# Kernel tuning notes

Measured on AMD Instinct MI355X. Metric: run time of the kernel, lower is better.

Reference implementation:

```python
import jax, jax.numpy as jnp
import numpy as np

HEADS = 8
DIM_HEAD = 64
DIM = 512
EPS = 1e-7  # module's self.eps, also used as LayerNorm eps


def _per_head_layernorm(t, w, b):
    # t: [b, h, n, d]; w, b: [h, d] (one LayerNorm per head, affine)
    mu = t.mean(axis=-1, keepdims=True)
    var = t.var(axis=-1, keepdims=True)  # biased, matches torch LayerNorm
    tn = (t - mu) * jax.lax.rsqrt(var + EPS)
    return tn * w[None, :, None, :] + b[None, :, None, :]


def setup_inputs() -> dict:
    key = jax.random.key(0)
    ks = jax.random.split(key, 4)
    inner = HEADS * DIM_HEAD
    return {
        "x": jax.random.normal(ks[0], (2, 2048, DIM), dtype=jnp.float32),
        "w_qkv": jax.random.normal(ks[1], (3 * inner, DIM), dtype=jnp.float32) * 0.02,
        "lnk_w": jnp.ones((HEADS, DIM_HEAD), dtype=jnp.float32),
        "lnk_b": jnp.zeros((HEADS, DIM_HEAD), dtype=jnp.float32),
        "lnv_w": jnp.ones((HEADS, DIM_HEAD), dtype=jnp.float32),
        "lnv_b": jnp.zeros((HEADS, DIM_HEAD), dtype=jnp.float32),
        "w_out": jax.random.normal(ks[2], (DIM, inner), dtype=jnp.float32) * 0.02,
        "b_out": jnp.zeros((DIM,), dtype=jnp.float32),
    }


def reference(x, w_qkv, lnk_w, lnk_b, lnv_w, lnv_b, w_out, b_out):
    b, n, _ = x.shape
    qkv = x @ w_qkv.T  # [b, n, 3*inner]
    q, k, v = jnp.split(qkv, 3, axis=-1)

    def split_heads(t):  # [b, n, h*d] -> [b, h, n, d]
        return t.reshape(b, n, HEADS, DIM_HEAD).transpose(0, 2, 1, 3)

    q, k, v = map(split_heads, (q, k, v))

    # per-head LayerNorm over dim_head on k and v
    k = _per_head_layernorm(k, lnk_w, lnk_b)
    v = _per_head_layernorm(v, lnv_w, lnv_b)

    # causal linear attention: prefix sums of k and of k-v outer products
    k_cum = jnp.cumsum(k, axis=2)  # [b, h, n, d]
    # scores: [b, h, n, d, e] prefix sums of outer products, scaled by 1/seq_len
    scores = jnp.cumsum(jnp.einsum('bhnd,bhne->bhnde', k, v), axis=2) / n
    d_inv = 1.0 / jnp.einsum('bhnd,bhnd->bhn', k_cum + EPS, q)  # [b, h, n]
    out = jnp.einsum('bhnd,bhnde,bhn->bhne', q, scores, d_inv)  # [b, h, n, e]

    out = out.transpose(0, 2, 1, 3).reshape(b, n, HEADS * DIM_HEAD)  # b n (h e)
    return out @ w_out.T + b_out
```

## Files before the change

kernel.cpp:

```cpp
#include <hip/hip_runtime.h>

constexpr int Bb   = 2;
constexpr int Nn   = 2048;
constexpr int Hh   = 8;
constexpr int Dd   = 64;
constexpr int Mm   = Bb * Nn;
constexpr int TQKV = 1536;
constexpr int INNER = Hh * Dd;
constexpr int CH   = 64;
constexpr int NCH  = Nn / CH;
constexpr int CSZ  = Dd * Dd + Dd;
constexpr float EPSF = 1e-7f;

typedef _Float16 half8 __attribute__((ext_vector_type(8)));
typedef _Float16 half4 __attribute__((ext_vector_type(4)));
typedef float f32x4 __attribute__((ext_vector_type(4)));

#define AS1(p) ((const __attribute__((address_space(1))) unsigned int*)(p))
#define AS3(p) ((__attribute__((address_space(3))) unsigned int*)(p))

__global__ __launch_bounds__(256) void gemm1_f32(
    const float* __restrict__ A, const float* __restrict__ B,
    float* __restrict__ C) {
  __shared__ float As[32][132];
  __shared__ float Bs[32][68];
  const int tid = threadIdx.x;
  const int tx = tid & 15, ty = tid >> 4;
  const int bm = blockIdx.y * 128, bn = blockIdx.x * 64;
  const int rowA = tid & 127, c4a = tid >> 7;
  const int rowB = tid & 63,  c4b = tid >> 6;

  float acc[8][4] = {};

  for (int k0 = 0; k0 < 512; k0 += 32) {
#pragma unroll
    for (int p = 0; p < 4; ++p) {
      int c4 = c4a + 2 * p;
      float4 fa = *(const float4*)(A + (size_t)(bm + rowA) * 512 + k0 + c4 * 4);
      As[c4 * 4 + 0][rowA] = fa.x; As[c4 * 4 + 1][rowA] = fa.y;
      As[c4 * 4 + 2][rowA] = fa.z; As[c4 * 4 + 3][rowA] = fa.w;
    }
#pragma unroll
    for (int p = 0; p < 2; ++p) {
      int c4 = c4b + 4 * p;
      float4 fb = *(const float4*)(B + (size_t)(bn + rowB) * 512 + k0 + c4 * 4);
      Bs[c4 * 4 + 0][rowB] = fb.x; Bs[c4 * 4 + 1][rowB] = fb.y;
      Bs[c4 * 4 + 2][rowB] = fb.z; Bs[c4 * 4 + 3][rowB] = fb.w;
    }
    __syncthreads();
#pragma unroll
    for (int kk = 0; kk < 32; ++kk) {
      float a[8], b[4];
      *(float4*)&a[0] = *(const float4*)&As[kk][ty * 8];
      *(float4*)&a[4] = *(const float4*)&As[kk][ty * 8 + 4];
      *(float4*)&b[0] = *(const float4*)&Bs[kk][tx * 4];
#pragma unroll
      for (int i = 0; i < 8; ++i)
#pragma unroll
        for (int j = 0; j < 4; ++j) acc[i][j] += a[i] * b[j];
    }
    __syncthreads();
  }

#pragma unroll
  for (int i = 0; i < 8; ++i) {
    size_t row = bm + ty * 8 + i;
    float4 r;
    r.x = acc[i][0]; r.y = acc[i][1]; r.z = acc[i][2]; r.w = acc[i][3];
    *(float4*)(C + row * (size_t)TQKV + bn + tx * 4) = r;
  }
}

__global__ __launch_bounds__(256) void split_f16_k(
    const float* __restrict__ s, _Float16* __restrict__ hi,
    _Float16* __restrict__ lo, int n4) {
  int i = blockIdx.x * 256 + threadIdx.x;
  if (i >= n4) return;
  float4 a = ((const float4*)s)[i];
  half4 h, l;
  float av[4] = {a.x, a.y, a.z, a.w};
#pragma unroll
  for (int j = 0; j < 4; ++j) {
    _Float16 hh = (_Float16)av[j];
    h[j] = hh;
    l[j] = (_Float16)((av[j] - (float)hh) * 2048.0f);
  }
  ((half4*)hi)[i] = h;
  ((half4*)lo)[i] = l;
}

__global__ __launch_bounds__(256) void gemm_split_nt(
    const _Float16* __restrict__ Ah, const _Float16* __restrict__ Al,
    const _Float16* __restrict__ Bh, const _Float16* __restrict__ Bl,
    const float* __restrict__ bias, float* __restrict__ C,
    int Ndim, int Kd) {
  constexpr int BM = 128, BN = 64, BK = 32;
  __shared__ _Float16 lds[(2 * BM + 2 * BN) * BK];
  constexpr int AHo = 0;
  constexpr int ALo = BM * BK;
  constexpr int BHo = 2 * BM * BK;
  constexpr int BLo = 2 * BM * BK + BN * BK;

  const int tid = threadIdx.x;
  const int wave = tid >> 6, lane = tid & 63;
  const int lq = lane >> 4, lm = lane & 15;
  const int bm = blockIdx.y * BM, bn = blockIdx.x * BN;

  f32x4 acc[2][4] = {};
  f32x4 corr[2][4] = {};

  const int nsteps = Kd >> 5;
  for (int ks = 0; ks < nsteps; ++ks) {
    const int k0 = ks * BK;
    for (int idx = wave; idx < 24; idx += 4) {
      int t, j;
      if (idx < 8)       { t = 0; j = idx; }
      else if (idx < 16) { t = 1; j = idx - 8; }
      else if (idx < 20) { t = 2; j = idx - 16; }
      else               { t = 3; j = idx - 20; }
      const int row = j * 16 + (lane >> 2);
      const _Float16* g;
      _Float16* l;
      if (t == 0)      { g = Ah + (size_t)(bm + row) * Kd; l = lds + AHo + j * 16 * BK; }
      else if (t == 1) { g = Al + (size_t)(bm + row) * Kd; l = lds + ALo + j * 16 * BK; }
      else if (t == 2) { g = Bh + (size_t)(bn + row) * Kd; l = lds + BHo + j * 16 * BK; }
      else             { g = Bl + (size_t)(bn + row) * Kd; l = lds + BLo + j * 16 * BK; }
      g += k0 + (lane & 3) * 8;
      __builtin_amdgcn_global_load_lds(AS1(g), AS3(l), 16, 0, 0);
    }
    __syncthreads();

    half8 ahf[2], alf[2], bhf[4], blf[4];
    const int mwo = wave * 32;
#pragma unroll
    for (int fi = 0; fi < 2; ++fi) {
      ahf[fi] = *(const half8*)&lds[AHo + (mwo + fi * 16 + lm) * BK + lq * 8];
      alf[fi] = *(const half8*)&lds[ALo + (mwo + fi * 16 + lm) * BK + lq * 8];
    }
#pragma unroll
    for (int fj = 0; fj < 4; ++fj) {
      bhf[fj] = *(const half8*)&lds[BHo + (fj * 16 + lm) * BK + lq * 8];
      blf[fj] = *(const half8*)&lds[BLo + (fj * 16 + lm) * BK + lq * 8];
    }
#pragma unroll
    for (int fi = 0; fi < 2; ++fi)
#pragma unroll
      for (int fj = 0; fj < 4; ++fj) {
        acc[fi][fj] = __builtin_amdgcn_mfma_f32_16x16x32_f16(
            ahf[fi], bhf[fj], acc[fi][fj], 0, 0, 0);
        corr[fi][fj] = __builtin_amdgcn_mfma_f32_16x16x32_f16(
            ahf[fi], blf[fj], corr[fi][fj], 0, 0, 0);
        corr[fi][fj] = __builtin_amdgcn_mfma_f32_16x16x32_f16(
            alf[fi], bhf[fj], corr[fi][fj], 0, 0, 0);
      }
    __syncthreads();
  }

#pragma unroll
  for (int fi = 0; fi < 2; ++fi) {
    const int m0 = bm + wave * 32 + fi * 16 + lq * 4;
#pragma unroll
    for (int fj = 0; fj < 4; ++fj) {
      const int n = bn + fj * 16 + lm;
      const float bb = bias ? bias[n] : 0.f;
      f32x4 v = acc[fi][fj];
      f32x4 cv = corr[fi][fj];
#pragma unroll
      for (int r = 0; r < 4; ++r)
        C[(size_t)(m0 + r) * Ndim + n] = v[r] + cv[r] * (1.0f / 2048.0f) + bb;
    }
  }
}

__global__ __launch_bounds__(256) void chunk_sums_ln(
    float* __restrict__ qkv, const float* __restrict__ lnk_w,
    const float* __restrict__ lnk_b, const float* __restrict__ lnv_w,
    const float* __restrict__ lnv_b, float* __restrict__ cbuf) {
  int blk = blockIdx.x;
  int c = blk % NCH;
  int bh = blk / NCH;
  int h = bh % Hh, b = bh / Hh;
  __shared__ float Ks[CH][68];
  __shared__ float Vs[CH][68];
  int tid = threadIdx.x;
  float* base = qkv + (size_t)(b * Nn + c * CH) * TQKV + h * Dd;
  for (int i = tid; i < CH * 16; i += 256) {
    int row = i >> 4, c4 = i & 15;
    *(float4*)&Ks[row][c4 * 4] =
        *(const float4*)(base + (size_t)row * TQKV + INNER + c4 * 4);
    *(float4*)&Vs[row][c4 * 4] =
        *(const float4*)(base + (size_t)row * TQKV + 2 * INNER + c4 * 4);
  }
  __syncthreads();

  if (tid < 128) {
    bool isv = tid >= 64;
    int row = tid & 63;
    float* R = isv ? &Vs[row][0] : &Ks[row][0];
    float s = 0.f, s2 = 0.f;
#pragma unroll
    for (int j = 0; j < 64; j += 4) {
      float4 v = *(const float4*)&R[j];
      s += v.x + v.y + v.z + v.w;
      s2 += v.x * v.x + v.y * v.y + v.z * v.z + v.w * v.w;
    }
    float mean = s * (1.f / 64.f);
    float var = s2 * (1.f / 64.f) - mean * mean;
    float inv = 1.0f / sqrtf(var + EPSF);
    const float* w = isv ? lnv_w : lnk_w;
    const float* bb = isv ? lnv_b : lnk_b;
#pragma unroll
    for (int j = 0; j < 64; ++j)
      R[j] = (R[j] - mean) * inv * w[h * Dd + j] + bb[h * Dd + j];
  }
  __syncthreads();

  for (int i = tid; i < CH * 16; i += 256) {
    int row = i >> 4, c4 = i & 15;
    *(float4*)(base + (size_t)row * TQKV + INNER + c4 * 4) =
        *(const float4*)&Ks[row][c4 * 4];
    *(float4*)(base + (size_t)row * TQKV + 2 * INNER + c4 * 4) =
        *(const float4*)&Vs[row][c4 * 4];
  }

  int d0 = (tid >> 4) * 4, e0 = (tid & 15) * 4;
  float acc[4][4] = {};
  float kc[4] = {0.f, 0.f, 0.f, 0.f};
  for (int n = 0; n < CH; ++n) {
    float4 kv = *(const float4*)&Ks[n][d0];
    float4 vv = *(const float4*)&Vs[n][e0];
    float ka[4] = {kv.x, kv.y, kv.z, kv.w};
    float va[4] = {vv.x, vv.y, vv.z, vv.w};
#pragma unroll
    for (int i = 0; i < 4; ++i)
#pragma unroll
      for (int j = 0; j < 4; ++j) acc[i][j] += ka[i] * va[j];
    if (e0 == 0) {
#pragma unroll
      for (int i = 0; i < 4; ++i) kc[i] += ka[i];
    }
  }
  float* out = cbuf + (size_t)blk * CSZ;
#pragma unroll
  for (int i = 0; i < 4; ++i) {
    float4 r;
    r.x = acc[i][0]; r.y = acc[i][1]; r.z = acc[i][2]; r.w = acc[i][3];
    *(float4*)(out + (size_t)(d0 + i) * Dd + e0) = r;
  }
  if (e0 == 0) {
#pragma unroll
    for (int i = 0; i < 4; ++i) out[Dd * Dd + d0 + i] = kc[i];
  }
}

__global__ __launch_bounds__(256) void chunk_prefix(float* __restrict__ cbuf) {
  int bh = blockIdx.y;
  int i = blockIdx.x * 256 + threadIdx.x;
  if (i >= CSZ) return;
  float* p = cbuf + (size_t)bh * NCH * CSZ + i;
  float carry = 0.f;
  for (int c = 0; c < NCH; ++c) {
    float t = p[(size_t)c * CSZ];
    p[(size_t)c * CSZ] = carry;
    carry += t;
  }
}

__global__ __launch_bounds__(256) void chunk_attn(
    const float* __restrict__ qkv, const float* __restrict__ cbuf,
    _Float16* __restrict__ atth, _Float16* __restrict__ attl) {
  int blk = blockIdx.x;
  int c = blk % NCH;
  int bh = blk / NCH;
  int h = bh % Hh, b = bh / Hh;
  __shared__ float Qs[64][68];
  __shared__ float Ks[64][68];
  __shared__ float Vs[64][68];
  __shared__ float Ss[64][68];
  __shared__ float kcs[64];
  __shared__ float rs[64][17];
  __shared__ float denomS[64];
  float (*Ps)[68] = Ks;

  int tid = threadIdx.x;
  int tx = tid & 15, ty = tid >> 4;
  const float* base = qkv + (size_t)(b * Nn + c * CH) * TQKV + h * Dd;
  for (int i = tid; i < CH * 16; i += 256) {
    int row = i >> 4, c4 = i & 15;
    float4 fq = *(const float4*)(base + (size_t)row * TQKV + c4 * 4);
    Qs[c4 * 4 + 0][row] = fq.x; Qs[c4 * 4 + 1][row] = fq.y;
    Qs[c4 * 4 + 2][row] = fq.z; Qs[c4 * 4 + 3][row] = fq.w;
    float4 fk = *(const float4*)(base + (size_t)row * TQKV + INNER + c4 * 4);
    Ks[c4 * 4 + 0][row] = fk.x; Ks[c4 * 4 + 1][row] = fk.y;
    Ks[c4 * 4 + 2][row] = fk.z; Ks[c4 * 4 + 3][row] = fk.w;
    float4 fv = *(const float4*)(base + (size_t)row * TQKV + 2 * INNER + c4 * 4);
    *(float4*)&Vs[row][c4 * 4] = fv;
  }
  const float* sp = cbuf + (size_t)blk * CSZ;
  for (int i = tid; i < 1024; i += 256) {
    int row = i >> 4;
    *(float4*)&Ss[row][(i & 15) * 4] = *(const float4*)(sp + (size_t)i * 4);
  }
  if (tid < 16) {
    float4 f = *(const float4*)(sp + Dd * Dd + tid * 4);
    kcs[tid * 4 + 0] = f.x; kcs[tid * 4 + 1] = f.y;
    kcs[tid * 4 + 2] = f.z; kcs[tid * 4 + 3] = f.w;
  }
  __syncthreads();

  float accP[4][4] = {};
  for (int kk = 0; kk < 64; ++kk) {
    float4 qa = *(const float4*)&Qs[kk][ty * 4];
    float4 kb = *(const float4*)&Ks[kk][tx * 4];
    float qv[4] = {qa.x, qa.y, qa.z, qa.w};
    float kv[4] = {kb.x, kb.y, kb.z, kb.w};
#pragma unroll
    for (int i = 0; i < 4; ++i)
#pragma unroll
      for (int j = 0; j < 4; ++j) accP[i][j] += qv[i] * kv[j];
  }
  __syncthreads();

#pragma unroll
  for (int i = 0; i < 4; ++i) {
    int n = ty * 4 + i;
    float rsum = 0.f;
#pragma unroll
    for (int j = 0; j < 4; ++j) {
      int m = tx * 4 + j;
      float p = (m <= n) ? accP[i][j] : 0.f;
      Ps[m][n] = p;
      rsum += p;
    }
    rs[n][tx] = rsum;
  }
  __syncthreads();

  float accO[4][4] = {};
  for (int d = 0; d < 64; ++d) {
    float4 qa = *(const float4*)&Qs[d][ty * 4];
    float4 sb = *(const float4*)&Ss[d][tx * 4];
    float qv[4] = {qa.x, qa.y, qa.z, qa.w};
    float sv[4] = {sb.x, sb.y, sb.z, sb.w};
#pragma unroll
    for (int i = 0; i < 4; ++i)
#pragma unroll
      for (int j = 0; j < 4; ++j) accO[i][j] += qv[i] * sv[j];
  }
  if (tid < 64) {
    int n = tid;
    float qkc = 0.f, qs = 0.f;
    for (int d = 0; d < 64; ++d) {
      float q = Qs[d][n];
      qkc += q * kcs[d];
      qs += q;
    }
    float rsum = 0.f;
#pragma unroll
    for (int t2 = 0; t2 < 16; ++t2) rsum += rs[n][t2];
    denomS[n] = qkc + rsum + EPSF * qs;
  }
  __syncthreads();

  for (int m = 0; m < 64; ++m) {
    float4 pa = *(const float4*)&Ps[m][ty * 4];
    float4 vb = *(const float4*)&Vs[m][tx * 4];
    float pv[4] = {pa.x, pa.y, pa.z, pa.w};
    float vv[4] = {vb.x, vb.y, vb.z, vb.w};
#pragma unroll
    for (int i = 0; i < 4; ++i)
#pragma unroll
      for (int j = 0; j < 4; ++j) accO[i][j] += pv[i] * vv[j];
  }

  size_t obase = (size_t)(b * Nn + c * CH) * INNER + h * Dd;
#pragma unroll
  for (int i = 0; i < 4; ++i) {
    int n = ty * 4 + i;
    float dinv = 1.0f / denomS[n];
    float scale = dinv * (1.0f / (float)Nn);
    half4 hv, lv;
#pragma unroll
    for (int j = 0; j < 4; ++j) {
      float o = accO[i][j] * scale;
      _Float16 hh = (_Float16)o;
      hv[j] = hh;
      lv[j] = (_Float16)((o - (float)hh) * 2048.0f);
    }
    *(half4*)(atth + obase + (size_t)n * INNER + tx * 4) = hv;
    *(half4*)(attl + obase + (size_t)n * INNER + tx * 4) = lv;
  }
}

extern "C" void kernel_launch(void* const* d_in, const int* in_sizes, int n_in,
                              void* d_out, int out_size, void* d_ws,
                              size_t ws_size, hipStream_t stream) {
  const float* x     = (const float*)d_in[0];
  const float* w_qkv = (const float*)d_in[1];
  const float* lnk_w = (const float*)d_in[2];
  const float* lnk_b = (const float*)d_in[3];
  const float* lnv_w = (const float*)d_in[4];
  const float* lnv_b = (const float*)d_in[5];
  const float* w_out = (const float*)d_in[6];
  const float* b_out = (const float*)d_in[7];
  float* out = (float*)d_out;

  float* qkv  = (float*)d_ws;
  float* cbuf = qkv + (size_t)Mm * TQKV;
  _Float16* atth = (_Float16*)(cbuf + (size_t)Bb * Hh * NCH * CSZ);
  _Float16* attl = atth + (size_t)Mm * INNER;
  _Float16* woh  = attl + (size_t)Mm * INNER;
  _Float16* wol  = woh + (size_t)INNER * 512;
  _Float16* xh   = wol + (size_t)INNER * 512;
  _Float16* xl   = xh + (size_t)Mm * 512;
  _Float16* wvh  = xl + (size_t)Mm * 512;
  _Float16* wvl  = wvh + (size_t)INNER * 512;

  split_f16_k<<<2048, 256, 0, stream>>>(x, xh, xl, Mm * 512 / 4);
  split_f16_k<<<256, 256, 0, stream>>>(
      w_qkv + (size_t)1024 * 512, wvh, wvl, INNER * 512 / 4);

  gemm1_f32<<<dim3(1024 / 64, Mm / 128), 256, 0, stream>>>(x, w_qkv, qkv);

  gemm_split_nt<<<dim3(512 / 64, Mm / 128), 256, 0, stream>>>(
      xh, xl, wvh, wvl, nullptr, qkv + 1024, TQKV, 512);

  chunk_sums_ln<<<Bb * Hh * NCH, 256, 0, stream>>>(
      qkv, lnk_w, lnk_b, lnv_w, lnv_b, cbuf);

  chunk_prefix<<<dim3((CSZ + 255) / 256, Bb * Hh), 256, 0, stream>>>(cbuf);

  split_f16_k<<<256, 256, 0, stream>>>(w_out, woh, wol, INNER * 512 / 4);

  chunk_attn<<<Bb * Hh * NCH, 256, 0, stream>>>(qkv, cbuf, atth, attl);

  gemm_split_nt<<<dim3(INNER / 64, Mm / 128), 256, 0, stream>>>(
      atth, attl, woh, wol, b_out, out, INNER, 512);
}
```

Before: 234.5 us.

## Fuse per-head LayerNorm of K and V into QKV GEMM epilogues

Moves the per-head LayerNorm on K and V out of the chunk-sum kernel and into the epilogues of the GEMMs that produce them. A 64-column output tile maps exactly to one head, so each block stages its tile in shared memory, computes row mean and inverse std, and writes normalized values once. This removes the extra read-modify-write of K and V through global memory in chunk_sums. The cost is a larger shared pool, an extra epilogue with two syncs in the GEMMs, and possibly lower occupancy.

```diff
diff --git a/kernel.cpp b/kernel.cpp
--- a/kernel.cpp
+++ b/kernel.cpp
@@ -21,9 +21,12 @@
 
 __global__ __launch_bounds__(256) void gemm1_f32(
     const float* __restrict__ A, const float* __restrict__ B,
-    float* __restrict__ C) {
-  __shared__ float As[32][132];
-  __shared__ float Bs[32][68];
+    float* __restrict__ C,
+    const float* __restrict__ lnk_w, const float* __restrict__ lnk_b) {
+  __shared__ float pool[8704];
+  __shared__ float mean_s[128], inv_s[128];
+  float* As = pool;
+  float* Bs = pool + 4224;
   const int tid = threadIdx.x;
   const int tx = tid & 15, ty = tid >> 4;
   const int bm = blockIdx.y * 128, bn = blockIdx.x * 64;
@@ -37,23 +40,23 @@
     for (int p = 0; p < 4; ++p) {
       int c4 = c4a + 2 * p;
       float4 fa = *(const float4*)(A + (size_t)(bm + rowA) * 512 + k0 + c4 * 4);
-      As[c4 * 4 + 0][rowA] = fa.x; As[c4 * 4 + 1][rowA] = fa.y;
-      As[c4 * 4 + 2][rowA] = fa.z; As[c4 * 4 + 3][rowA] = fa.w;
+      As[(c4 * 4 + 0) * 132 + rowA] = fa.x; As[(c4 * 4 + 1) * 132 + rowA] = fa.y;
+      As[(c4 * 4 + 2) * 132 + rowA] = fa.z; As[(c4 * 4 + 3) * 132 + rowA] = fa.w;
     }
 #pragma unroll
     for (int p = 0; p < 2; ++p) {
       int c4 = c4b + 4 * p;
       float4 fb = *(const float4*)(B + (size_t)(bn + rowB) * 512 + k0 + c4 * 4);
-      Bs[c4 * 4 + 0][rowB] = fb.x; Bs[c4 * 4 + 1][rowB] = fb.y;
-      Bs[c4 * 4 + 2][rowB] = fb.z; Bs[c4 * 4 + 3][rowB] = fb.w;
+      Bs[(c4 * 4 + 0) * 68 + rowB] = fb.x; Bs[(c4 * 4 + 1) * 68 + rowB] = fb.y;
+      Bs[(c4 * 4 + 2) * 68 + rowB] = fb.z; Bs[(c4 * 4 + 3) * 68 + rowB] = fb.w;
     }
     __syncthreads();
 #pragma unroll
     for (int kk = 0; kk < 32; ++kk) {
       float a[8], b[4];
-      *(float4*)&a[0] = *(const float4*)&As[kk][ty * 8];
-      *(float4*)&a[4] = *(const float4*)&As[kk][ty * 8 + 4];
-      *(float4*)&b[0] = *(const float4*)&Bs[kk][tx * 4];
+      *(float4*)&a[0] = *(const float4*)&As[kk * 132 + ty * 8];
+      *(float4*)&a[4] = *(const float4*)&As[kk * 132 + ty * 8 + 4];
+      *(float4*)&b[0] = *(const float4*)&Bs[kk * 68 + tx * 4];
 #pragma unroll
       for (int i = 0; i < 8; ++i)
 #pragma unroll
@@ -62,12 +65,50 @@
     __syncthreads();
   }
 
-#pragma unroll
-  for (int i = 0; i < 8; ++i) {
-    size_t row = bm + ty * 8 + i;
-    float4 r;
-    r.x = acc[i][0]; r.y = acc[i][1]; r.z = acc[i][2]; r.w = acc[i][3];
-    *(float4*)(C + row * (size_t)TQKV + bn + tx * 4) = r;
+  if (bn < 512) {
+#pragma unroll
+    for (int i = 0; i < 8; ++i) {
+      size_t row = bm + ty * 8 + i;
+      float4 r;
+      r.x = acc[i][0]; r.y = acc[i][1]; r.z = acc[i][2]; r.w = acc[i][3];
+      *(float4*)(C + row * (size_t)TQKV + bn + tx * 4) = r;
+    }
+  } else {
+#pragma unroll
+    for (int i = 0; i < 8; ++i)
+#pragma unroll
+      for (int j = 0; j < 4; ++j)
+        pool[(ty * 8 + i) * 68 + tx * 4 + j] = acc[i][j];
+    __syncthreads();
+    if (tid < 128) {
+      const float* R = pool + tid * 68;
+      float s = 0.f, s2 = 0.f;
+#pragma unroll
+      for (int j = 0; j < 64; j += 4) {
+        float4 v = *(const float4*)&R[j];
+        s += v.x + v.y + v.z + v.w;
+        s2 += v.x * v.x + v.y * v.y + v.z * v.z + v.w * v.w;
+      }
+      float mean = s * (1.f / 64.f);
+      float var = s2 * (1.f / 64.f) - mean * mean;
+      mean_s[tid] = mean;
+      inv_s[tid] = 1.0f / sqrtf(var + EPSF);
+    }
+    __syncthreads();
+    const int h = (bn - 512) >> 6;
+    for (int i = tid; i < 128 * 16; i += 256) {
+      int row = i >> 4, c4 = i & 15;
+      float4 v = *(const float4*)&pool[row * 68 + c4 * 4];
+      float4 w = *(const float4*)(lnk_w + h * 64 + c4 * 4);
+      float4 bb = *(const float4*)(lnk_b + h * 64 + c4 * 4);
+      float m = mean_s[row], iv = inv_s[row];
+      float4 r;
+      r.x = (v.x - m) * iv * w.x + bb.x;
+      r.y = (v.y - m) * iv * w.y + bb.y;
+      r.z = (v.z - m) * iv * w.z + bb.z;
+      r.w = (v.w - m) * iv * w.w + bb.w;
+      *(float4*)(C + (size_t)(bm + row) * TQKV + bn + c4 * 4) = r;
+    }
   }
 }
 
@@ -93,9 +134,12 @@
     const _Float16* __restrict__ Ah, const _Float16* __restrict__ Al,
     const _Float16* __restrict__ Bh, const _Float16* __restrict__ Bl,
     const float* __restrict__ bias, float* __restrict__ C,
-    int Ndim, int Kd) {
+    int Ndim, int Kd,
+    const float* __restrict__ lnw, const float* __restrict__ lnb) {
   constexpr int BM = 128, BN = 64, BK = 32;
-  __shared__ _Float16 lds[(2 * BM + 2 * BN) * BK];
+  __shared__ float pool[8704];
+  __shared__ float mean_s[128], inv_s[128];
+  _Float16* lds = (_Float16*)pool;
   constexpr int AHo = 0;
   constexpr int ALo = BM * BK;
   constexpr int BHo = 2 * BM * BK;
@@ -156,26 +200,70 @@
     __syncthreads();
   }
 
-#pragma unroll
-  for (int fi = 0; fi < 2; ++fi) {
-    const int m0 = bm + wave * 32 + fi * 16 + lq * 4;
-#pragma unroll
-    for (int fj = 0; fj < 4; ++fj) {
-      const int n = bn + fj * 16 + lm;
-      const float bb = bias ? bias[n] : 0.f;
-      f32x4 v = acc[fi][fj];
-      f32x4 cv = corr[fi][fj];
-#pragma unroll
-      for (int r = 0; r < 4; ++r)
-        C[(size_t)(m0 + r) * Ndim + n] = v[r] + cv[r] * (1.0f / 2048.0f) + bb;
-    }
-  }
-}
-
-__global__ __launch_bounds__(256) void chunk_sums_ln(
-    float* __restrict__ qkv, const float* __restrict__ lnk_w,
-    const float* __restrict__ lnk_b, const float* __restrict__ lnv_w,
-    const float* __restrict__ lnv_b, float* __restrict__ cbuf) {
+  if (!lnw) {
+#pragma unroll
+    for (int fi = 0; fi < 2; ++fi) {
+      const int m0 = bm + wave * 32 + fi * 16 + lq * 4;
+#pragma unroll
+      for (int fj = 0; fj < 4; ++fj) {
+        const int n = bn + fj * 16 + lm;
+        const float bb = bias ? bias[n] : 0.f;
+        f32x4 v = acc[fi][fj];
+        f32x4 cv = corr[fi][fj];
+#pragma unroll
+        for (int r = 0; r < 4; ++r)
+          C[(size_t)(m0 + r) * Ndim + n] = v[r] + cv[r] * (1.0f / 2048.0f) + bb;
+      }
+    }
+  } else {
+#pragma unroll
+    for (int fi = 0; fi < 2; ++fi) {
+      const int r0 = wave * 32 + fi * 16 + lq * 4;
+#pragma unroll
+      for (int fj = 0; fj < 4; ++fj) {
+        const int n = fj * 16 + lm;
+        f32x4 v = acc[fi][fj];
+        f32x4 cv = corr[fi][fj];
+#pragma unroll
+        for (int r = 0; r < 4; ++r)
+          pool[(r0 + r) * 68 + n] = v[r] + cv[r] * (1.0f / 2048.0f);
+      }
+    }
+    __syncthreads();
+    if (tid < 128) {
+      const float* R = pool + tid * 68;
+      float s = 0.f, s2 = 0.f;
+#pragma unroll
+      for (int j = 0; j < 64; j += 4) {
+        float4 v = *(const float4*)&R[j];
+        s += v.x + v.y + v.z + v.w;
+        s2 += v.x * v.x + v.y * v.y + v.z * v.z + v.w * v.w;
+      }
+      float mean = s * (1.f / 64.f);
+      float var = s2 * (1.f / 64.f) - mean * mean;
+      mean_s[tid] = mean;
+      inv_s[tid] = 1.0f / sqrtf(var + EPSF);
+    }
+    __syncthreads();
+    const int h = bn >> 6;
+    for (int i = tid; i < 128 * 16; i += 256) {
+      int row = i >> 4, c4 = i & 15;
+      float4 v = *(const float4*)&pool[row * 68 + c4 * 4];
+      float4 w = *(const float4*)(lnw + h * 64 + c4 * 4);
+      float4 bb = *(const float4*)(lnb + h * 64 + c4 * 4);
+      float m = mean_s[row], iv = inv_s[row];
+      float4 r;
+      r.x = (v.x - m) * iv * w.x + bb.x;
+      r.y = (v.y - m) * iv * w.y + bb.y;
+      r.z = (v.z - m) * iv * w.z + bb.z;
+      r.w = (v.w - m) * iv * w.w + bb.w;
+      *(float4*)(C + (size_t)(bm + row) * Ndim + bn + c4 * 4) = r;
+    }
+  }
+}
+
+__global__ __launch_bounds__(256) void chunk_sums(
+    const float* __restrict__ qkv, float* __restrict__ cbuf) {
   int blk = blockIdx.x;
   int c = blk % NCH;
   int bh = blk / NCH;
@@ -183,7 +271,7 @@
   __shared__ float Ks[CH][68];
   __shared__ float Vs[CH][68];
   int tid = threadIdx.x;
-  float* base = qkv + (size_t)(b * Nn + c * CH) * TQKV + h * Dd;
+  const float* base = qkv + (size_t)(b * Nn + c * CH) * TQKV + h * Dd;
   for (int i = tid; i < CH * 16; i += 256) {
     int row = i >> 4, c4 = i & 15;
     *(float4*)&Ks[row][c4 * 4] =
@@ -192,37 +280,6 @@
         *(const float4*)(base + (size_t)row * TQKV + 2 * INNER + c4 * 4);
   }
   __syncthreads();
-
-  if (tid < 128) {
-    bool isv = tid >= 64;
-    int row = tid & 63;
-    float* R = isv ? &Vs[row][0] : &Ks[row][0];
-    float s = 0.f, s2 = 0.f;
-#pragma unroll
-    for (int j = 0; j < 64; j += 4) {
-      float4 v = *(const float4*)&R[j];
-      s += v.x + v.y + v.z + v.w;
-      s2 += v.x * v.x + v.y * v.y + v.z * v.z + v.w * v.w;
-    }
-    float mean = s * (1.f / 64.f);
-    float var = s2 * (1.f / 64.f) - mean * mean;
-    float inv = 1.0f / sqrtf(var + EPSF);
-    const float* w = isv ? lnv_w : lnk_w;
-    const float* bb = isv ? lnv_b : lnk_b;
-#pragma unroll
-    for (int j = 0; j < 64; ++j)
-      R[j] = (R[j] - mean) * inv * w[h * Dd + j] + bb[h * Dd + j];
-  }
-  __syncthreads();
-
-  for (int i = tid; i < CH * 16; i += 256) {
-    int row = i >> 4, c4 = i & 15;
-    *(float4*)(base + (size_t)row * TQKV + INNER + c4 * 4) =
-        *(const float4*)&Ks[row][c4 * 4];
-    *(float4*)(base + (size_t)row * TQKV + 2 * INNER + c4 * 4) =
-        *(const float4*)&Vs[row][c4 * 4];
-  }
-
   int d0 = (tid >> 4) * 4, e0 = (tid & 15) * 4;
   float acc[4][4] = {};
   float kc[4] = {0.f, 0.f, 0.f, 0.f};
@@ -420,13 +477,13 @@
   split_f16_k<<<256, 256, 0, stream>>>(
       w_qkv + (size_t)1024 * 512, wvh, wvl, INNER * 512 / 4);
 
-  gemm1_f32<<<dim3(1024 / 64, Mm / 128), 256, 0, stream>>>(x, w_qkv, qkv);
+  gemm1_f32<<<dim3(1024 / 64, Mm / 128), 256, 0, stream>>>(
+      x, w_qkv, qkv, lnk_w, lnk_b);
 
   gemm_split_nt<<<dim3(512 / 64, Mm / 128), 256, 0, stream>>>(
-      xh, xl, wvh, wvl, nullptr, qkv + 1024, TQKV, 512);
-
-  chunk_sums_ln<<<Bb * Hh * NCH, 256, 0, stream>>>(
-      qkv, lnk_w, lnk_b, lnv_w, lnv_b, cbuf);
+      xh, xl, wvh, wvl, nullptr, qkv + 1024, TQKV, 512, lnv_w, lnv_b);
+
+  chunk_sums<<<Bb * Hh * NCH, 256, 0, stream>>>(qkv, cbuf);
 
   chunk_prefix<<<dim3((CSZ + 255) / 256, Bb * Hh), 256, 0, stream>>>(cbuf);
 
@@ -435,5 +492,5 @@
   chunk_attn<<<Bb * Hh * NCH, 256, 0, stream>>>(qkv, cbuf, atth, attl);
 
   gemm_split_nt<<<dim3(INNER / 64, Mm / 128), 256, 0, stream>>>(
-      atth, attl, woh, wol, b_out, out, INNER, 512);
-}
+      atth, attl, woh, wol, b_out, out, INNER, 512, nullptr, nullptr);
+}
```

Result: no change. 236.0 us (+0.6%).
